# Kernel tuning notes

Hardware: AMD Instinct MI355X
Metric: run time of the kernel (lower is better)

Reference implementation:

```python
import jax, jax.numpy as jnp
import numpy as np

B, C, H, W = 2048, 4, 84, 84
FEAT = 7 * 7 * 64  # 3136, from 84->20->9->7 conv arithmetic
D = 512
E = 6            # num_experts
K = 2            # top_k
A = 12           # output_dim (actions)


def _conv(x, w, b, stride):
    y = jax.lax.conv_general_dilated(
        x, w, window_strides=(stride, stride), padding='VALID',
        dimension_numbers=('NCHW', 'OIHW', 'NCHW'))
    return y + b[None, :, None, None]


def setup_inputs() -> dict:
    key = jax.random.key(0)
    ks = jax.random.split(key, 16)
    s = lambda k, shape, fan: jax.random.normal(k, shape, jnp.float32) * (1.0 / np.sqrt(fan))
    return {
        'x': jax.random.normal(ks[0], (B, C, H, W), jnp.float32),
        'c1_w': s(ks[1], (32, C, 8, 8), C * 64), 'c1_b': jnp.zeros((32,), jnp.float32),
        'c2_w': s(ks[2], (64, 32, 4, 4), 32 * 16), 'c2_b': jnp.zeros((64,), jnp.float32),
        'c3_w': s(ks[3], (64, 64, 3, 3), 64 * 9), 'c3_b': jnp.zeros((64,), jnp.float32),
        'fc_w': s(ks[4], (FEAT, D), FEAT), 'fc_b': jnp.zeros((D,), jnp.float32),
        'gate_w': s(ks[5], (D, E), D), 'gate_b': jnp.zeros((E,), jnp.float32),
        'e_w1': s(ks[6], (E, D, D), D), 'e_b1': jnp.zeros((E, D), jnp.float32),
        'e_w2': s(ks[7], (E, D, D), D), 'e_b2': jnp.zeros((E, D), jnp.float32),
        'e_w3': s(ks[8], (E, D, A), D), 'e_b3': jnp.zeros((E, A), jnp.float32),
    }


def reference(x, c1_w, c1_b, c2_w, c2_b, c3_w, c3_b, fc_w, fc_b,
              gate_w, gate_b, e_w1, e_b1, e_w2, e_b2, e_w3, e_b3):
    # CNN feature extractor (dropout omitted: eval semantics)
    h = jax.nn.relu(_conv(x, c1_w, c1_b, 4))
    h = jax.nn.relu(_conv(h, c2_w, c2_b, 2))
    h = jax.nn.relu(_conv(h, c3_w, c3_b, 1))
    h = h.reshape(h.shape[0], -1)                     # [B, 3136] (C,H,W flatten order)
    f = jax.nn.relu(h @ fc_w + fc_b)                  # [B, 512]

    # Gating: softmax -> top-2 -> renormalize
    gate_probs = jax.nn.softmax(f @ gate_w + gate_b, axis=-1)    # [B, E]
    top_p, top_i = jax.lax.top_k(gate_probs, K)                   # [B, K]
    top_p = top_p / jnp.sum(top_p, axis=-1, keepdims=True)

    # Experts: compute all (tiny MLPs), then gather top-k outputs
    h1 = jax.nn.relu(jnp.einsum('bd,edh->beh', f, e_w1) + e_b1)   # [B, E, D]
    h2 = jax.nn.relu(jnp.einsum('beh,ehg->beg', h1, e_w2) + e_b2) # [B, E, D]
    eo = jnp.einsum('beg,ego->beo', h2, e_w3) + e_b3              # [B, E, A]
    sel = jnp.take_along_axis(eo, top_i[:, :, None], axis=1)      # [B, K, A]
    out = jnp.sum(sel * top_p[:, :, None], axis=1)                # [B, A]
    return out
```

## Files before the change

### kernel.cpp

```cpp
#include <hip/hip_runtime.h>
#include <hip/hip_bf16.h>
#include <math.h>

typedef __attribute__((ext_vector_type(8))) short bf16x8;
typedef __attribute__((ext_vector_type(4))) float f32x4;

__device__ __forceinline__ float b2f(unsigned short u) {
    unsigned int v = ((unsigned int)u) << 16;
    return __uint_as_float(v);
}
__device__ __forceinline__ unsigned short f2b(float f) {
    __hip_bfloat16 h = __float2bfloat16(f);
    return *reinterpret_cast<unsigned short*>(&h);
}
__device__ __forceinline__ void split_trunc(float v, short& h, short& l) {
    unsigned int ui = __float_as_uint(v);
    h = (short)(ui >> 16);
    float hf = __uint_as_float(ui & 0xffff0000u);
    l = (short)f2b(v - hf);
}

__global__ __launch_bounds__(256) void prep_all(
    const float* __restrict__ w1, const float* __restrict__ w2, const float* __restrict__ w3,
    const float* __restrict__ ew3, const float* __restrict__ fw,
    const float* __restrict__ ew1, const float* __restrict__ ew2,
    unsigned short* __restrict__ wb1h, unsigned short* __restrict__ wb1l,
    unsigned short* __restrict__ w2h, unsigned short* __restrict__ w2l,
    unsigned short* __restrict__ w3h, unsigned short* __restrict__ w3l,
    float* __restrict__ w3t,
    unsigned short* __restrict__ fh, unsigned short* __restrict__ fl,
    unsigned short* __restrict__ t1, unsigned short* __restrict__ t2) {
    __shared__ float lds_f[64 * 65];
    int b = blockIdx.x;
    int t = threadIdx.x;
    if (b < 448) {
        int tid = b * 256 + t;
        if (tid < 8192) {
            int k = tid >> 8, r = tid & 255;
            int c = r >> 6, ky = (r >> 3) & 7, kx = r & 7;
            float v = w1[tid];
            unsigned short h = f2b(v);
            int d = ((ky * 2 + (k >> 4)) * 16 + (k & 15)) * 32 + c * 8 + kx;
            wb1h[d] = h;
            wb1l[d] = f2b(v - b2f(h));
        } else if (tid < 8192 + 32768) {
            int i = tid - 8192;
            int n = i >> 9, r = i & 511;
            int c = r >> 4, ky = (r >> 2) & 3, kx = r & 3;
            float v = w2[i];
            unsigned short h = f2b(v);
            int d = ((ky * 4 + kx) * 64 + n) * 32 + c;
            w2h[d] = h;
            w2l[d] = f2b(v - b2f(h));
        } else if (tid < 8192 + 32768 + 36864) {
            int i = tid - 40960;
            int n = i / 576, r = i - n * 576;
            int c = r / 9, s = r - c * 9;
            int ky = s / 3, kx = s - ky * 3;
            float v = w3[i];
            unsigned short h = f2b(v);
            int d = (((ky * 3 + kx) * 2 + (c >> 5)) * 64 + n) * 32 + (c & 31);
            w3h[d] = h;
            w3l[d] = f2b(v - b2f(h));
        } else if (tid < 77824 + 36864) {
            int i = tid - 77824;
            int e = i / 6144, rem = i - e * 6144;
            int a = rem >> 9, k = rem & 511;
            w3t[i] = ew3[e * 6144 + k * 12 + a];
        }
    } else if (b < 840) {
        int bx = b - 448;
        int k0 = (bx % 49) * 64;
        int n0 = (bx / 49) * 64;
        int tx = t & 63, ty = t >> 6;
#pragma unroll
        for (int j = 0; j < 16; j++) {
            int kk = ty + j * 4;
            int kp = k0 + kk;
            int p = kp >> 6, c = kp & 63;
            lds_f[kk * 65 + tx] = fw[(c * 49 + p) * 512 + n0 + tx];
        }
        __syncthreads();
#pragma unroll
        for (int j = 0; j < 16; j++) {
            int r = ty + j * 4;
            float v = lds_f[tx * 65 + r];
            unsigned short hh = f2b(v);
            long d = (long)(n0 + r) * 3136 + k0 + tx;
            fh[d] = hh;
            fl[d] = f2b(v - b2f(hh));
        }
    } else {
        int i = b - 840;
        int h0 = (i & 15) * 32;
        int d0 = ((i >> 4) & 15) * 32;
        int z = i >> 8;
        int e = z % 6;
        const float* src = (z < 6) ? (ew1 + e * 262144) : (ew2 + e * 262144);
        unsigned short* dst = (z < 6) ? (t1 + e * 262144) : (t2 + e * 262144);
        int tx = t & 31, ty = t >> 5;
#pragma unroll
        for (int j = 0; j < 4; j++)
            lds_f[(ty + j * 8) * 33 + tx] = src[(d0 + ty + j * 8) * 512 + h0 + tx];
        __syncthreads();
#pragma unroll
        for (int j = 0; j < 4; j++)
            dst[(h0 + ty + j * 8) * 512 + (d0 + tx)] = f2b(lds_f[tx * 33 + ty + j * 8]);
    }
}

__global__ __launch_bounds__(256, 4) void conv1_k(
    const float* __restrict__ x, const unsigned short* __restrict__ wbh,
    const unsigned short* __restrict__ wbl, const float* __restrict__ b1,
    unsigned short* __restrict__ yhi, unsigned short* __restrict__ ylo) {
    __shared__ bf16x8 wlds[8][4][64];
    int t = threadIdx.x;
    {
        int tab = t >> 6, ln = t & 63;
        const unsigned short* sb = ((tab < 2) ? wbh : wbl) +
            ((ln & 15) * 32 + (ln >> 4) * 8 + (tab & 1) * 512);
#pragma unroll
        for (int k = 0; k < 8; k++)
            wlds[k][tab][ln] = *(const bf16x8*)(sb + k * 1024);
    }
    int swz = (blockIdx.x & 7) * 800 + (blockIdx.x >> 3);
    int wave = t >> 6, lane = t & 63, l16 = lane & 15, quad = lane >> 4;
    int px0 = swz * 128 + wave * 32;
    const float* abase[2];
#pragma unroll
    for (int i = 0; i < 2; i++) {
        int px = px0 + i * 16 + l16;
        int n = px / 400;
        int rem = px - n * 400;
        int oy = rem / 20;
        int ox = rem - oy * 20;
        abase[i] = x + (long)n * 28224 + quad * 7056 + oy * 4 * 84 + ox * 4;
    }
    f32x4 acc[2][2];
#pragma unroll
    for (int i = 0; i < 2; i++)
#pragma unroll
        for (int j = 0; j < 2; j++)
#pragma unroll
            for (int r = 0; r < 4; r++) acc[i][j][r] = 0.f;
    __syncthreads();
    float4 buf[4][4];
#pragma unroll
    for (int r = 0; r < 3; r++) {
        __builtin_amdgcn_sched_barrier(0);
#pragma unroll
        for (int i = 0; i < 2; i++) {
            const float* p = abase[i] + r * 84;
            buf[r][i * 2] = *(const float4*)p;
            buf[r][i * 2 + 1] = *(const float4*)(p + 4);
        }
        __builtin_amdgcn_sched_barrier(0);
    }
#pragma unroll
    for (int ky = 0; ky < 8; ky++) {
        if (ky < 5) {
            __builtin_amdgcn_sched_barrier(0);
#pragma unroll
            for (int i = 0; i < 2; i++) {
                const float* p = abase[i] + (ky + 3) * 84;
                buf[(ky + 3) & 3][i * 2] = *(const float4*)p;
                buf[(ky + 3) & 3][i * 2 + 1] = *(const float4*)(p + 4);
            }
            __builtin_amdgcn_sched_barrier(0);
        }
        bf16x8 bh0 = wlds[ky][0][lane];
        bf16x8 bh1 = wlds[ky][1][lane];
        bf16x8 bl0 = wlds[ky][2][lane];
        bf16x8 bl1 = wlds[ky][3][lane];
        bf16x8 ah[2], al[2];
#pragma unroll
        for (int i = 0; i < 2; i++) {
            const float4& c0 = buf[ky & 3][i * 2];
            const float4& c1 = buf[ky & 3][i * 2 + 1];
            float v[8] = {c0.x, c0.y, c0.z, c0.w, c1.x, c1.y, c1.z, c1.w};
#pragma unroll
            for (int j = 0; j < 8; j++) {
                short hh, ll;
                split_trunc(v[j], hh, ll);
                ah[i][j] = hh;
                al[i][j] = ll;
            }
        }
#pragma unroll
        for (int i = 0; i < 2; i++) {
            acc[i][0] = __builtin_amdgcn_mfma_f32_16x16x32_bf16(ah[i], bh0, acc[i][0], 0, 0, 0);
            acc[i][0] = __builtin_amdgcn_mfma_f32_16x16x32_bf16(al[i], bh0, acc[i][0], 0, 0, 0);
            acc[i][0] = __builtin_amdgcn_mfma_f32_16x16x32_bf16(ah[i], bl0, acc[i][0], 0, 0, 0);
            acc[i][1] = __builtin_amdgcn_mfma_f32_16x16x32_bf16(ah[i], bh1, acc[i][1], 0, 0, 0);
            acc[i][1] = __builtin_amdgcn_mfma_f32_16x16x32_bf16(al[i], bh1, acc[i][1], 0, 0, 0);
            acc[i][1] = __builtin_amdgcn_mfma_f32_16x16x32_bf16(ah[i], bl1, acc[i][1], 0, 0, 0);
        }
    }
    float bias0 = b1[l16], bias1 = b1[16 + l16];
#pragma unroll
    for (int i = 0; i < 2; i++) {
#pragma unroll
        for (int r = 0; r < 4; r++) {
            long px = px0 + i * 16 + quad * 4 + r;
            long o = px * 32;
            float v0 = fmaxf(acc[i][0][r] + bias0, 0.f);
            float v1 = fmaxf(acc[i][1][r] + bias1, 0.f);
            short h0, l0, h1, l1;
            split_trunc(v0, h0, l0);
            split_trunc(v1, h1, l1);
            yhi[o + l16] = (unsigned short)h0;
            ylo[o + l16] = (unsigned short)l0;
            yhi[o + 16 + l16] = (unsigned short)h1;
            ylo[o + 16 + l16] = (unsigned short)l1;
        }
    }
}

template <int C, int IH, int IW, int OH, int OW, int S, int KH, int KW>
__global__ __launch_bounds__(256, 2) void convm_k(
    const unsigned short* __restrict__ xhi, const unsigned short* __restrict__ xlo,
    const unsigned short* __restrict__ whi, const unsigned short* __restrict__ wlo,
    const float* __restrict__ bias,
    unsigned short* __restrict__ yhi, unsigned short* __restrict__ ylo) {
    constexpr int CH = C / 32;
    constexpr int NCHUNK = KH * KW * CH;
    __shared__ unsigned short Bst[2][2][4][64][8];
    int t = threadIdx.x;
    int wave = t >> 6, lane = t & 63, l16 = lane & 15, quad = lane >> 4;
    int pxbase = blockIdx.x * 256 + wave * 64;
    long xoff[4];
#pragma unroll
    for (int i = 0; i < 4; i++) {
        int px = pxbase + i * 16 + l16;
        int n = px / (OH * OW);
        int rem = px - n * (OH * OW);
        int oy = rem / OW;
        int ox = rem - oy * OW;
        xoff[i] = (((long)n * IH + oy * S) * IW + ox * S) * C + quad * 8;
    }
    f32x4 acc[4][4];
#pragma unroll
    for (int i = 0; i < 4; i++)
#pragma unroll
        for (int j = 0; j < 4; j++)
#pragma unroll
            for (int r = 0; r < 4; r++) acc[i][j][r] = 0.f;
    long wsrc = (long)lane * 32 + wave * 8;
    uint4 sh = *(const uint4*)(whi + wsrc);
    uint4 sl = *(const uint4*)(wlo + wsrc);
    bf16x8 a_h[4], a_l[4];
    {
#pragma unroll
        for (int i = 0; i < 4; i++) {
            a_h[i] = *(const bf16x8*)(xhi + xoff[i]);
            a_l[i] = *(const bf16x8*)(xlo + xoff[i]);
        }
    }
    *(uint4*)&Bst[0][0][wave][lane][0] = sh;
    *(uint4*)&Bst[0][1][wave][lane][0] = sl;
    asm volatile("s_waitcnt lgkmcnt(0)\n\ts_barrier" ::: "memory");
#pragma unroll
    for (int ck = 0; ck < NCHUNK; ck++) {
        const int cur = ck & 1;
        uint4 nsh, nsl;
        bf16x8 na_h[4], na_l[4];
        if (ck + 1 < NCHUNK) {
            long ws = (long)(ck + 1) * 2048 + lane * 32 + wave * 8;
            nsh = *(const uint4*)(whi + ws);
            nsl = *(const uint4*)(wlo + ws);
            int ck1 = ck + 1;
            int kyx = ck1 / CH;
            int ch = ck1 - kyx * CH;
            int ky = kyx / KW, kx = kyx - ky * KW;
            long k1 = ((long)(ky * IW + kx)) * C + ch * 32;
#pragma unroll
            for (int i = 0; i < 4; i++) {
                na_h[i] = *(const bf16x8*)(xhi + xoff[i] + k1);
                na_l[i] = *(const bf16x8*)(xlo + xoff[i] + k1);
            }
        }
        bf16x8 bh[4], bl[4];
#pragma unroll
        for (int j = 0; j < 4; j++) {
            bh[j] = *(const bf16x8*)&Bst[cur][0][quad][j * 16 + l16][0];
            bl[j] = *(const bf16x8*)&Bst[cur][1][quad][j * 16 + l16][0];
        }
#pragma unroll
        for (int i = 0; i < 4; i++)
#pragma unroll
            for (int j = 0; j < 4; j++) {
                acc[i][j] = __builtin_amdgcn_mfma_f32_16x16x32_bf16(a_h[i], bh[j], acc[i][j], 0, 0, 0);
                acc[i][j] = __builtin_amdgcn_mfma_f32_16x16x32_bf16(a_h[i], bl[j], acc[i][j], 0, 0, 0);
                acc[i][j] = __builtin_amdgcn_mfma_f32_16x16x32_bf16(a_l[i], bh[j], acc[i][j], 0, 0, 0);
            }
        if (ck + 1 < NCHUNK) {
            __builtin_amdgcn_sched_barrier(0);
            *(uint4*)&Bst[cur ^ 1][0][wave][lane][0] = nsh;
            *(uint4*)&Bst[cur ^ 1][1][wave][lane][0] = nsl;
            asm volatile("s_waitcnt lgkmcnt(0)\n\ts_barrier" ::: "memory");
#pragma unroll
            for (int i = 0; i < 4; i++) {
                a_h[i] = na_h[i];
                a_l[i] = na_l[i];
            }
        }
    }
#pragma unroll
    for (int i = 0; i < 4; i++)
#pragma unroll
        for (int j = 0; j < 4; j++) {
            int col = j * 16 + l16;
            float bv = bias[col];
#pragma unroll
            for (int r = 0; r < 4; r++) {
                int prow = pxbase + i * 16 + quad * 4 + r;
                float v = fmaxf(acc[i][j][r] + bv, 0.f);
                unsigned short h = f2b(v);
                yhi[(long)prow * 64 + col] = h;
                ylo[(long)prow * 64 + col] = f2b(v - b2f(h));
            }
        }
}

__global__ __launch_bounds__(64, 3) void fc_k(
    const unsigned short* __restrict__ Ahi, const unsigned short* __restrict__ Alo,
    const unsigned short* __restrict__ Bhi, const unsigned short* __restrict__ Blo,
    float* __restrict__ Cp, int* __restrict__ cnt) {
    if (blockIdx.x == 0 && blockIdx.y == 0 && blockIdx.z == 0 && threadIdx.x < 8)
        cnt[threadIdx.x] = 0;
    int lane = threadIdx.x, l16 = lane & 15, quad = lane >> 4;
    int m0 = blockIdx.x * 64, n0 = blockIdx.y * 64;
    int z = blockIdx.z;
    int kBase = z * 448;
    f32x4 acc[4][4];
#pragma unroll
    for (int i = 0; i < 4; i++)
#pragma unroll
        for (int j = 0; j < 4; j++)
#pragma unroll
            for (int r = 0; r < 4; r++) acc[i][j][r] = 0.f;
#pragma unroll 2
    for (int k0 = kBase; k0 < kBase + 448; k0 += 32) {
        bf16x8 ah[4], al[4], bh[4], bl[4];
#pragma unroll
        for (int i = 0; i < 4; i++) {
            long a = (long)(m0 + i * 16 + l16) * 3136 + k0 + quad * 8;
            ah[i] = *(const bf16x8*)(Ahi + a);
            al[i] = *(const bf16x8*)(Alo + a);
        }
#pragma unroll
        for (int j = 0; j < 4; j++) {
            long b = (long)(n0 + j * 16 + l16) * 3136 + k0 + quad * 8;
            bh[j] = *(const bf16x8*)(Bhi + b);
            bl[j] = *(const bf16x8*)(Blo + b);
        }
#pragma unroll
        for (int i = 0; i < 4; i++)
#pragma unroll
            for (int j = 0; j < 4; j++) {
                acc[i][j] = __builtin_amdgcn_mfma_f32_16x16x32_bf16(ah[i], bh[j], acc[i][j], 0, 0, 0);
                acc[i][j] = __builtin_amdgcn_mfma_f32_16x16x32_bf16(ah[i], bl[j], acc[i][j], 0, 0, 0);
                acc[i][j] = __builtin_amdgcn_mfma_f32_16x16x32_bf16(al[i], bh[j], acc[i][j], 0, 0, 0);
            }
    }
    float* Cz = Cp + (long)z * 1048576;
#pragma unroll
    for (int i = 0; i < 4; i++)
#pragma unroll
        for (int j = 0; j < 4; j++) {
            int col = n0 + j * 16 + l16;
#pragma unroll
            for (int r = 0; r < 4; r++) {
                int row = m0 + i * 16 + quad * 4 + r;
                Cz[row * 512 + col] = acc[i][j][r];
            }
        }
}

__global__ __launch_bounds__(256) void fin_gate(
    const float* __restrict__ Cp, const float* __restrict__ bias,
    const float* __restrict__ gw, const float* __restrict__ gb,
    unsigned short* __restrict__ fb, int* __restrict__ topi, float* __restrict__ topp,
    int* __restrict__ cnt, int* __restrict__ rowlist, int* __restrict__ slotp) {
    __shared__ float frow[512];
    int row = blockIdx.x;
    int t = threadIdx.x;
#pragma unroll
    for (int s = 0; s < 2; s++) {
        int c = t + s * 256;
        long base = (long)row * 512 + c;
        float v = bias[c];
#pragma unroll
        for (int z = 0; z < 7; z++) v += Cp[base + (long)z * 1048576];
        v = fmaxf(v, 0.f);
        fb[base] = f2b(v);
        frow[c] = v;
    }
    __syncthreads();
    if (t < 64) {
        int lane = t;
        float fv[8];
#pragma unroll
        for (int j = 0; j < 8; j++) fv[j] = frow[lane + 64 * j];
        float lg[6];
#pragma unroll
        for (int e = 0; e < 6; e++) {
            float a = 0.f;
#pragma unroll
            for (int j = 0; j < 8; j++) a += fv[j] * gw[(lane + 64 * j) * 6 + e];
#pragma unroll
            for (int off = 32; off > 0; off >>= 1) a += __shfl_xor(a, off, 64);
            lg[e] = a + gb[e];
        }
        if (lane == 0) {
            int i1 = 0;
            float v1 = lg[0];
#pragma unroll
            for (int e = 1; e < 6; e++)
                if (lg[e] > v1) { v1 = lg[e]; i1 = e; }
            int i2 = (i1 == 0) ? 1 : 0;
            float v2 = lg[i2];
#pragma unroll
            for (int e = 0; e < 6; e++)
                if (e != i1 && lg[e] > v2) { v2 = lg[e]; i2 = e; }
            float pa = 1.f / (1.f + expf(v2 - v1));
            topi[row * 2] = i1;
            topi[row * 2 + 1] = i2;
            topp[row * 2] = pa;
            topp[row * 2 + 1] = 1.f - pa;
            int s1 = atomicAdd(cnt + i1, 1);
            int s2 = atomicAdd(cnt + i2, 1);
            rowlist[i1 * 2048 + s1] = row;
            rowlist[i2 * 2048 + s2] = row;
            slotp[row * 2] = s1;
            slotp[row * 2 + 1] = s2;
        }
    }
}

__global__ __launch_bounds__(64, 4) void moe_gemm(
    const unsigned short* __restrict__ A, long aStride,
    const unsigned short* __restrict__ Bt, const float* __restrict__ bias,
    unsigned short* __restrict__ C,
    const int* __restrict__ cnt, const int* __restrict__ rowlist) {
    int e = blockIdx.z;
    int ne = cnt[e];
    int m0 = blockIdx.x * 64;
    if (m0 >= ne) return;
    const unsigned short* Ae = A + (long)e * aStride;
    const unsigned short* Be = Bt + (long)e * 262144;
    const float* be = bias + e * 512;
    unsigned short* Ce = C + (long)e * 2048 * 512;
    int lane = threadIdx.x, l16 = lane & 15, quad = lane >> 4;
    int n0 = blockIdx.y * 64;
    int arow[4];
#pragma unroll
    for (int i = 0; i < 4; i++) {
        int slot = m0 + i * 16 + l16;
        arow[i] = rowlist ? ((slot < ne) ? rowlist[e * 2048 + slot] : 0) : slot;
    }
    f32x4 acc[4][4];
#pragma unroll
    for (int i = 0; i < 4; i++)
#pragma unroll
        for (int j = 0; j < 4; j++)
#pragma unroll
            for (int r = 0; r < 4; r++) acc[i][j][r] = 0.f;
#pragma unroll 4
    for (int k0 = 0; k0 < 512; k0 += 32) {
        bf16x8 a[4], b[4];
#pragma unroll
        for (int i = 0; i < 4; i++)
            a[i] = *(const bf16x8*)(Ae + (long)arow[i] * 512 + k0 + quad * 8);
#pragma unroll
        for (int j = 0; j < 4; j++)
            b[j] = *(const bf16x8*)(Be + (long)(n0 + j * 16 + l16) * 512 + k0 + quad * 8);
#pragma unroll
        for (int i = 0; i < 4; i++)
#pragma unroll
            for (int j = 0; j < 4; j++)
                acc[i][j] = __builtin_amdgcn_mfma_f32_16x16x32_bf16(a[i], b[j], acc[i][j], 0, 0, 0);
    }
#pragma unroll
    for (int i = 0; i < 4; i++)
#pragma unroll
        for (int j = 0; j < 4; j++) {
            int col = n0 + j * 16 + l16;
            float bcol = be[col];
#pragma unroll
            for (int r = 0; r < 4; r++) {
                int row = m0 + i * 16 + quad * 4 + r;
                float v = fmaxf(acc[i][j][r] + bcol, 0.f);
                Ce[(long)row * 512 + col] = f2b(v);
            }
        }
}

__global__ __launch_bounds__(256) void combine_k(
    const unsigned short* __restrict__ h2, const float* __restrict__ w3t,
    const float* __restrict__ b3, const int* __restrict__ topi,
    const float* __restrict__ topp, const int* __restrict__ slotp,
    float* __restrict__ out) {
    int b = blockIdx.x * 4 + (threadIdx.x >> 6);
    int lane = threadIdx.x & 63;
    int e0 = topi[b * 2], e1 = topi[b * 2 + 1];
    float p0 = topp[b * 2], p1 = topp[b * 2 + 1];
    int s0 = slotp[b * 2], s1 = slotp[b * 2 + 1];
    float r[12];
#pragma unroll
    for (int a = 0; a < 12; a++) r[a] = 0.f;
#pragma unroll
    for (int j = 0; j < 2; j++) {
        int e = j ? e1 : e0;
        int s = j ? s1 : s0;
        float p = j ? p1 : p0;
        const unsigned short* hp = h2 + ((long)e * 2048 + s) * 512 + lane * 8;
        bf16x8 hv = *(const bf16x8*)hp;
        float hf[8];
#pragma unroll
        for (int q = 0; q < 8; q++) hf[q] = b2f((unsigned short)hv[q]);
        const float* wb = w3t + e * 6144 + lane * 8;
#pragma unroll
        for (int a = 0; a < 12; a++) {
            float4 w0 = *(const float4*)(wb + a * 512);
            float4 w1 = *(const float4*)(wb + a * 512 + 4);
            float acc = hf[0] * w0.x + hf[1] * w0.y + hf[2] * w0.z + hf[3] * w0.w +
                        hf[4] * w1.x + hf[5] * w1.y + hf[6] * w1.z + hf[7] * w1.w;
            r[a] += p * acc;
        }
    }
#pragma unroll
    for (int a = 0; a < 12; a++)
#pragma unroll
        for (int off = 32; off > 0; off >>= 1) r[a] += __shfl_xor(r[a], off, 64);
    float v = 0.f;
#pragma unroll
    for (int a = 0; a < 12; a++)
        if (lane == a) v = r[a];
    if (lane < 12)
        out[b * 12 + lane] = v + p0 * b3[e0 * 12 + lane] + p1 * b3[e1 * 12 + lane];
}

extern "C" void kernel_launch(void* const* d_in, const int* in_sizes, int n_in,
                              void* d_out, int out_size, void* d_ws, size_t ws_size,
                              hipStream_t stream) {
    const float* x   = (const float*)d_in[0];
    const float* c1w = (const float*)d_in[1];
    const float* c1b = (const float*)d_in[2];
    const float* c2w = (const float*)d_in[3];
    const float* c2b = (const float*)d_in[4];
    const float* c3w = (const float*)d_in[5];
    const float* c3b = (const float*)d_in[6];
    const float* fcw = (const float*)d_in[7];
    const float* fcb = (const float*)d_in[8];
    const float* gw  = (const float*)d_in[9];
    const float* gb  = (const float*)d_in[10];
    const float* ew1 = (const float*)d_in[11];
    const float* eb1 = (const float*)d_in[12];
    const float* ew2 = (const float*)d_in[13];
    const float* eb2 = (const float*)d_in[14];
    const float* ew3 = (const float*)d_in[15];
    const float* eb3 = (const float*)d_in[16];

    char* ws = (char*)d_ws;
    unsigned short* y1hi = (unsigned short*)(ws + 0L);
    unsigned short* y1lo = (unsigned short*)(ws + 52428800L);
    unsigned short* f3hi = (unsigned short*)(ws + 0L);
    unsigned short* f3lo = (unsigned short*)(ws + 12845056L);
    int*   cnt           = (int*)(ws + 26214400L);
    int*   rowlist       = (int*)(ws + 26214464L);
    int*   slotp         = (int*)(ws + 26263616L);
    unsigned short* y2hi = (unsigned short*)(ws + 104857600L);
    unsigned short* y2lo = (unsigned short*)(ws + 126091264L);
    unsigned short* h1   = (unsigned short*)(ws + 104857600L);
    unsigned short* h2   = (unsigned short*)(ws + 117440512L);
    unsigned short* fb   = (unsigned short*)(ws + 151519232L);
    int*   topi          = (int*)(ws + 153616384L);
    float* topp          = (float*)(ws + 153632768L);
    unsigned short* w2h  = (unsigned short*)(ws + 153681920L);
    unsigned short* w2l  = (unsigned short*)(ws + 153747456L);
    unsigned short* w3h  = (unsigned short*)(ws + 153812992L);
    unsigned short* w3l  = (unsigned short*)(ws + 153886720L);
    unsigned short* fcwh = (unsigned short*)(ws + 153960448L);
    unsigned short* fcwl = (unsigned short*)(ws + 157171712L);
    unsigned short* ew1t = (unsigned short*)(ws + 160382976L);
    unsigned short* ew2t = (unsigned short*)(ws + 163528704L);
    float* w3t           = (float*)(ws + 166674432L);
    float* Cp            = (float*)(ws + 166821888L);
    unsigned short* wb1h = (unsigned short*)(ws + 196182016L);
    unsigned short* wb1l = (unsigned short*)(ws + 196198400L);
    float* out = (float*)d_out;

    hipLaunchKernelGGL(prep_all, dim3(3912), dim3(256), 0, stream,
                       c1w, c2w, c3w, ew3, fcw, ew1, ew2,
                       wb1h, wb1l, w2h, w2l, w3h, w3l, w3t, fcwh, fcwl, ew1t, ew2t);
    hipLaunchKernelGGL(conv1_k, dim3(6400), dim3(256), 0, stream, x, wb1h, wb1l, c1b, y1hi, y1lo);
    hipLaunchKernelGGL((convm_k<32, 20, 20, 9, 9, 2, 4, 4>), dim3(648), dim3(256), 0, stream,
                       y1hi, y1lo, w2h, w2l, c2b, y2hi, y2lo);
    hipLaunchKernelGGL((convm_k<64, 9, 9, 7, 7, 1, 3, 3>), dim3(392), dim3(256), 0, stream,
                       y2hi, y2lo, w3h, w3l, c3b, f3hi, f3lo);
    hipLaunchKernelGGL(fc_k, dim3(32, 8, 7), dim3(64), 0, stream, f3hi, f3lo, fcwh, fcwl, Cp, cnt);
    hipLaunchKernelGGL(fin_gate, dim3(2048), dim3(256), 0, stream, Cp, fcb, gw, gb,
                       fb, topi, topp, cnt, rowlist, slotp);
    hipLaunchKernelGGL(moe_gemm, dim3(32, 8, 6), dim3(64), 0, stream, fb, 0L, ew1t, eb1, h1,
                       cnt, rowlist);
    hipLaunchKernelGGL(moe_gemm, dim3(32, 8, 6), dim3(64), 0, stream, h1, 1048576L, ew2t, eb2, h2,
                       cnt, (const int*)nullptr);
    hipLaunchKernelGGL(combine_k, dim3(512), dim3(256), 0, stream, h2, w3t, eb3, topi, topp,
                       slotp, out);
}
```

Baseline: 685.9 us.

## Shrink conv/fc tiles to single-wave blocks with register double-buffered loads

The strided conv kernels change from 256-thread blocks that stage weights through shared memory behind barriers to 64-thread blocks that each compute 32 pixels and load both activations and weights straight into double-buffered registers. The fc GEMM tile drops from 64 to 32 rows, doubling its grid, and gets the same register double-buffering. moe_gemm also gets register prefetch of the next K slice, with its occupancy hint changed from 4 to 3. The aim is to remove block-wide barriers and raise parallelism and load/MFMA overlap, at the cost of more global traffic for weights, since they are no longer shared across waves, and higher register pressure.

New measurement: 739.2 us. +7.8%, slower.

```diff
diff --git a/kernel.cpp b/kernel.cpp
--- a/kernel.cpp
+++ b/kernel.cpp
@@ -217,20 +217,18 @@
 }
 
 template <int C, int IH, int IW, int OH, int OW, int S, int KH, int KW>
-__global__ __launch_bounds__(256, 2) void convm_k(
+__global__ __launch_bounds__(64, 3) void convm_k(
     const unsigned short* __restrict__ xhi, const unsigned short* __restrict__ xlo,
     const unsigned short* __restrict__ whi, const unsigned short* __restrict__ wlo,
     const float* __restrict__ bias,
     unsigned short* __restrict__ yhi, unsigned short* __restrict__ ylo) {
     constexpr int CH = C / 32;
     constexpr int NCHUNK = KH * KW * CH;
-    __shared__ unsigned short Bst[2][2][4][64][8];
-    int t = threadIdx.x;
-    int wave = t >> 6, lane = t & 63, l16 = lane & 15, quad = lane >> 4;
-    int pxbase = blockIdx.x * 256 + wave * 64;
-    long xoff[4];
-#pragma unroll
-    for (int i = 0; i < 4; i++) {
+    int lane = threadIdx.x, l16 = lane & 15, quad = lane >> 4;
+    int pxbase = blockIdx.x * 32;
+    long xoff[2];
+#pragma unroll
+    for (int i = 0; i < 2; i++) {
         int px = pxbase + i * 16 + l16;
         int n = px / (OH * OW);
         int rem = px - n * (OH * OW);
@@ -238,75 +236,59 @@
         int ox = rem - oy * OW;
         xoff[i] = (((long)n * IH + oy * S) * IW + ox * S) * C + quad * 8;
     }
-    f32x4 acc[4][4];
-#pragma unroll
-    for (int i = 0; i < 4; i++)
+    f32x4 acc[2][4];
+#pragma unroll
+    for (int i = 0; i < 2; i++)
 #pragma unroll
         for (int j = 0; j < 4; j++)
 #pragma unroll
             for (int r = 0; r < 4; r++) acc[i][j][r] = 0.f;
-    long wsrc = (long)lane * 32 + wave * 8;
-    uint4 sh = *(const uint4*)(whi + wsrc);
-    uint4 sl = *(const uint4*)(wlo + wsrc);
-    bf16x8 a_h[4], a_l[4];
-    {
-#pragma unroll
-        for (int i = 0; i < 4; i++) {
-            a_h[i] = *(const bf16x8*)(xhi + xoff[i]);
-            a_l[i] = *(const bf16x8*)(xlo + xoff[i]);
-        }
-    }
-    *(uint4*)&Bst[0][0][wave][lane][0] = sh;
-    *(uint4*)&Bst[0][1][wave][lane][0] = sl;
-    asm volatile("s_waitcnt lgkmcnt(0)\n\ts_barrier" ::: "memory");
+    bf16x8 Ah[2][2], Al[2][2], Bh[2][4], Bl[2][4];
+    __builtin_amdgcn_sched_barrier(0);
+#pragma unroll
+    for (int i = 0; i < 2; i++) {
+        Ah[0][i] = *(const bf16x8*)(xhi + xoff[i]);
+        Al[0][i] = *(const bf16x8*)(xlo + xoff[i]);
+    }
+#pragma unroll
+    for (int j = 0; j < 4; j++) {
+        Bh[0][j] = *(const bf16x8*)(whi + (long)(j * 16 + l16) * 32 + quad * 8);
+        Bl[0][j] = *(const bf16x8*)(wlo + (long)(j * 16 + l16) * 32 + quad * 8);
+    }
+    __builtin_amdgcn_sched_barrier(0);
 #pragma unroll
     for (int ck = 0; ck < NCHUNK; ck++) {
         const int cur = ck & 1;
-        uint4 nsh, nsl;
-        bf16x8 na_h[4], na_l[4];
         if (ck + 1 < NCHUNK) {
-            long ws = (long)(ck + 1) * 2048 + lane * 32 + wave * 8;
-            nsh = *(const uint4*)(whi + ws);
-            nsl = *(const uint4*)(wlo + ws);
-            int ck1 = ck + 1;
-            int kyx = ck1 / CH;
-            int ch = ck1 - kyx * CH;
-            int ky = kyx / KW, kx = kyx - ky * KW;
-            long k1 = ((long)(ky * IW + kx)) * C + ch * 32;
-#pragma unroll
-            for (int i = 0; i < 4; i++) {
-                na_h[i] = *(const bf16x8*)(xhi + xoff[i] + k1);
-                na_l[i] = *(const bf16x8*)(xlo + xoff[i] + k1);
-            }
-        }
-        bf16x8 bh[4], bl[4];
-#pragma unroll
-        for (int j = 0; j < 4; j++) {
-            bh[j] = *(const bf16x8*)&Bst[cur][0][quad][j * 16 + l16][0];
-            bl[j] = *(const bf16x8*)&Bst[cur][1][quad][j * 16 + l16][0];
-        }
-#pragma unroll
-        for (int i = 0; i < 4; i++)
+            const int c1 = ck + 1;
+            const int kyx = c1 / CH;
+            const int ch = c1 - kyx * CH;
+            const int ky = kyx / KW, kx = kyx - ky * KW;
+            const long k1 = ((long)(ky * IW + kx)) * C + ch * 32;
+            __builtin_amdgcn_sched_barrier(0);
+#pragma unroll
+            for (int i = 0; i < 2; i++) {
+                Ah[cur ^ 1][i] = *(const bf16x8*)(xhi + xoff[i] + k1);
+                Al[cur ^ 1][i] = *(const bf16x8*)(xlo + xoff[i] + k1);
+            }
 #pragma unroll
             for (int j = 0; j < 4; j++) {
-                acc[i][j] = __builtin_amdgcn_mfma_f32_16x16x32_bf16(a_h[i], bh[j], acc[i][j], 0, 0, 0);
-                acc[i][j] = __builtin_amdgcn_mfma_f32_16x16x32_bf16(a_h[i], bl[j], acc[i][j], 0, 0, 0);
-                acc[i][j] = __builtin_amdgcn_mfma_f32_16x16x32_bf16(a_l[i], bh[j], acc[i][j], 0, 0, 0);
-            }
-        if (ck + 1 < NCHUNK) {
-            __builtin_amdgcn_sched_barrier(0);
-            *(uint4*)&Bst[cur ^ 1][0][wave][lane][0] = nsh;
-            *(uint4*)&Bst[cur ^ 1][1][wave][lane][0] = nsl;
-            asm volatile("s_waitcnt lgkmcnt(0)\n\ts_barrier" ::: "memory");
-#pragma unroll
-            for (int i = 0; i < 4; i++) {
-                a_h[i] = na_h[i];
-                a_l[i] = na_l[i];
-            }
-        }
-    }
-#pragma unroll
-    for (int i = 0; i < 4; i++)
+                Bh[cur ^ 1][j] = *(const bf16x8*)(whi + ((long)c1 * 64 + j * 16 + l16) * 32 + quad * 8);
+                Bl[cur ^ 1][j] = *(const bf16x8*)(wlo + ((long)c1 * 64 + j * 16 + l16) * 32 + quad * 8);
+            }
+            __builtin_amdgcn_sched_barrier(0);
+        }
+#pragma unroll
+        for (int i = 0; i < 2; i++)
+#pragma unroll
+            for (int j = 0; j < 4; j++) {
+                acc[i][j] = __builtin_amdgcn_mfma_f32_16x16x32_bf16(Ah[cur][i], Bh[cur][j], acc[i][j], 0, 0, 0);
+                acc[i][j] = __builtin_amdgcn_mfma_f32_16x16x32_bf16(Ah[cur][i], Bl[cur][j], acc[i][j], 0, 0, 0);
+                acc[i][j] = __builtin_amdgcn_mfma_f32_16x16x32_bf16(Al[cur][i], Bh[cur][j], acc[i][j], 0, 0, 0);
+            }
+    }
+#pragma unroll
+    for (int i = 0; i < 2; i++)
 #pragma unroll
         for (int j = 0; j < 4; j++) {
             int col = j * 16 + l16;
@@ -329,43 +311,64 @@
     if (blockIdx.x == 0 && blockIdx.y == 0 && blockIdx.z == 0 && threadIdx.x < 8)
         cnt[threadIdx.x] = 0;
     int lane = threadIdx.x, l16 = lane & 15, quad = lane >> 4;
-    int m0 = blockIdx.x * 64, n0 = blockIdx.y * 64;
+    int m0 = blockIdx.x * 32, n0 = blockIdx.y * 64;
     int z = blockIdx.z;
     int kBase = z * 448;
-    f32x4 acc[4][4];
-#pragma unroll
-    for (int i = 0; i < 4; i++)
+    long aoff[2], boff[4];
+#pragma unroll
+    for (int i = 0; i < 2; i++) aoff[i] = (long)(m0 + i * 16 + l16) * 3136 + kBase + quad * 8;
+#pragma unroll
+    for (int j = 0; j < 4; j++) boff[j] = (long)(n0 + j * 16 + l16) * 3136 + kBase + quad * 8;
+    f32x4 acc[2][4];
+#pragma unroll
+    for (int i = 0; i < 2; i++)
 #pragma unroll
         for (int j = 0; j < 4; j++)
 #pragma unroll
             for (int r = 0; r < 4; r++) acc[i][j][r] = 0.f;
-#pragma unroll 2
-    for (int k0 = kBase; k0 < kBase + 448; k0 += 32) {
-        bf16x8 ah[4], al[4], bh[4], bl[4];
-#pragma unroll
-        for (int i = 0; i < 4; i++) {
-            long a = (long)(m0 + i * 16 + l16) * 3136 + k0 + quad * 8;
-            ah[i] = *(const bf16x8*)(Ahi + a);
-            al[i] = *(const bf16x8*)(Alo + a);
-        }
-#pragma unroll
-        for (int j = 0; j < 4; j++) {
-            long b = (long)(n0 + j * 16 + l16) * 3136 + k0 + quad * 8;
-            bh[j] = *(const bf16x8*)(Bhi + b);
-            bl[j] = *(const bf16x8*)(Blo + b);
-        }
-#pragma unroll
-        for (int i = 0; i < 4; i++)
+    bf16x8 Ah[2][2], Al[2][2], Bh[2][4], Bl[2][4];
+    __builtin_amdgcn_sched_barrier(0);
+#pragma unroll
+    for (int i = 0; i < 2; i++) {
+        Ah[0][i] = *(const bf16x8*)(Ahi + aoff[i]);
+        Al[0][i] = *(const bf16x8*)(Alo + aoff[i]);
+    }
+#pragma unroll
+    for (int j = 0; j < 4; j++) {
+        Bh[0][j] = *(const bf16x8*)(Bhi + boff[j]);
+        Bl[0][j] = *(const bf16x8*)(Blo + boff[j]);
+    }
+    __builtin_amdgcn_sched_barrier(0);
+#pragma unroll
+    for (int s = 0; s < 14; s++) {
+        const int cur = s & 1;
+        if (s + 1 < 14) {
+            const int k1 = (s + 1) * 32;
+            __builtin_amdgcn_sched_barrier(0);
+#pragma unroll
+            for (int i = 0; i < 2; i++) {
+                Ah[cur ^ 1][i] = *(const bf16x8*)(Ahi + aoff[i] + k1);
+                Al[cur ^ 1][i] = *(const bf16x8*)(Alo + aoff[i] + k1);
+            }
 #pragma unroll
             for (int j = 0; j < 4; j++) {
-                acc[i][j] = __builtin_amdgcn_mfma_f32_16x16x32_bf16(ah[i], bh[j], acc[i][j], 0, 0, 0);
-                acc[i][j] = __builtin_amdgcn_mfma_f32_16x16x32_bf16(ah[i], bl[j], acc[i][j], 0, 0, 0);
-                acc[i][j] = __builtin_amdgcn_mfma_f32_16x16x32_bf16(al[i], bh[j], acc[i][j], 0, 0, 0);
+                Bh[cur ^ 1][j] = *(const bf16x8*)(Bhi + boff[j] + k1);
+                Bl[cur ^ 1][j] = *(const bf16x8*)(Blo + boff[j] + k1);
+            }
+            __builtin_amdgcn_sched_barrier(0);
+        }
+#pragma unroll
+        for (int i = 0; i < 2; i++)
+#pragma unroll
+            for (int j = 0; j < 4; j++) {
+                acc[i][j] = __builtin_amdgcn_mfma_f32_16x16x32_bf16(Ah[cur][i], Bh[cur][j], acc[i][j], 0, 0, 0);
+                acc[i][j] = __builtin_amdgcn_mfma_f32_16x16x32_bf16(Ah[cur][i], Bl[cur][j], acc[i][j], 0, 0, 0);
+                acc[i][j] = __builtin_amdgcn_mfma_f32_16x16x32_bf16(Al[cur][i], Bh[cur][j], acc[i][j], 0, 0, 0);
             }
     }
     float* Cz = Cp + (long)z * 1048576;
 #pragma unroll
-    for (int i = 0; i < 4; i++)
+    for (int i = 0; i < 2; i++)
 #pragma unroll
         for (int j = 0; j < 4; j++) {
             int col = n0 + j * 16 + l16;
@@ -438,7 +441,7 @@
     }
 }
 
-__global__ __launch_bounds__(64, 4) void moe_gemm(
+__global__ __launch_bounds__(64, 3) void moe_gemm(
     const unsigned short* __restrict__ A, long aStride,
     const unsigned short* __restrict__ Bt, const float* __restrict__ bias,
     unsigned short* __restrict__ C,
@@ -453,12 +456,15 @@
     unsigned short* Ce = C + (long)e * 2048 * 512;
     int lane = threadIdx.x, l16 = lane & 15, quad = lane >> 4;
     int n0 = blockIdx.y * 64;
-    int arow[4];
+    long aoff[4], boff[4];
 #pragma unroll
     for (int i = 0; i < 4; i++) {
         int slot = m0 + i * 16 + l16;
-        arow[i] = rowlist ? ((slot < ne) ? rowlist[e * 2048 + slot] : 0) : slot;
-    }
+        int ar = rowlist ? ((slot < ne) ? rowlist[e * 2048 + slot] : 0) : slot;
+        aoff[i] = (long)ar * 512 + quad * 8;
+    }
+#pragma unroll
+    for (int j = 0; j < 4; j++) boff[j] = (long)(n0 + j * 16 + l16) * 512 + quad * 8;
     f32x4 acc[4][4];
 #pragma unroll
     for (int i = 0; i < 4; i++)
@@ -466,20 +472,30 @@
         for (int j = 0; j < 4; j++)
 #pragma unroll
             for (int r = 0; r < 4; r++) acc[i][j][r] = 0.f;
-#pragma unroll 4
-    for (int k0 = 0; k0 < 512; k0 += 32) {
-        bf16x8 a[4], b[4];
+    bf16x8 As[2][4], Bs[2][4];
+    __builtin_amdgcn_sched_barrier(0);
+#pragma unroll
+    for (int i = 0; i < 4; i++) As[0][i] = *(const bf16x8*)(Ae + aoff[i]);
+#pragma unroll
+    for (int j = 0; j < 4; j++) Bs[0][j] = *(const bf16x8*)(Be + boff[j]);
+    __builtin_amdgcn_sched_barrier(0);
+#pragma unroll
+    for (int s = 0; s < 16; s++) {
+        const int cur = s & 1;
+        if (s + 1 < 16) {
+            const int k1 = (s + 1) * 32;
+            __builtin_amdgcn_sched_barrier(0);
+#pragma unroll
+            for (int i = 0; i < 4; i++) As[cur ^ 1][i] = *(const bf16x8*)(Ae + aoff[i] + k1);
+#pragma unroll
+            for (int j = 0; j < 4; j++) Bs[cur ^ 1][j] = *(const bf16x8*)(Be + boff[j] + k1);
+            __builtin_amdgcn_sched_barrier(0);
+        }
 #pragma unroll
         for (int i = 0; i < 4; i++)
-            a[i] = *(const bf16x8*)(Ae + (long)arow[i] * 512 + k0 + quad * 8);
-#pragma unroll
-        for (int j = 0; j < 4; j++)
-            b[j] = *(const bf16x8*)(Be + (long)(n0 + j * 16 + l16) * 512 + k0 + quad * 8);
-#pragma unroll
-        for (int i = 0; i < 4; i++)
 #pragma unroll
             for (int j = 0; j < 4; j++)
-                acc[i][j] = __builtin_amdgcn_mfma_f32_16x16x32_bf16(a[i], b[j], acc[i][j], 0, 0, 0);
+                acc[i][j] = __builtin_amdgcn_mfma_f32_16x16x32_bf16(As[cur][i], Bs[cur][j], acc[i][j], 0, 0, 0);
     }
 #pragma unroll
     for (int i = 0; i < 4; i++)
@@ -595,11 +611,11 @@
                        c1w, c2w, c3w, ew3, fcw, ew1, ew2,
                        wb1h, wb1l, w2h, w2l, w3h, w3l, w3t, fcwh, fcwl, ew1t, ew2t);
     hipLaunchKernelGGL(conv1_k, dim3(6400), dim3(256), 0, stream, x, wb1h, wb1l, c1b, y1hi, y1lo);
-    hipLaunchKernelGGL((convm_k<32, 20, 20, 9, 9, 2, 4, 4>), dim3(648), dim3(256), 0, stream,
+    hipLaunchKernelGGL((convm_k<32, 20, 20, 9, 9, 2, 4, 4>), dim3(5184), dim3(64), 0, stream,
                        y1hi, y1lo, w2h, w2l, c2b, y2hi, y2lo);
-    hipLaunchKernelGGL((convm_k<64, 9, 9, 7, 7, 1, 3, 3>), dim3(392), dim3(256), 0, stream,
+    hipLaunchKernelGGL((convm_k<64, 9, 9, 7, 7, 1, 3, 3>), dim3(3136), dim3(64), 0, stream,
                        y2hi, y2lo, w3h, w3l, c3b, f3hi, f3lo);
-    hipLaunchKernelGGL(fc_k, dim3(32, 8, 7), dim3(64), 0, stream, f3hi, f3lo, fcwh, fcwl, Cp, cnt);
+    hipLaunchKernelGGL(fc_k, dim3(64, 8, 7), dim3(64), 0, stream, f3hi, f3lo, fcwh, fcwl, Cp, cnt);
     hipLaunchKernelGGL(fin_gate, dim3(2048), dim3(256), 0, stream, Cp, fcb, gw, gb,
                        fb, topi, topp, cnt, rowlist, slotp);
     hipLaunchKernelGGL(moe_gemm, dim3(32, 8, 6), dim3(64), 0, stream, fb, 0L, ew1t, eb1, h1,
```
